# Optimization experiments

Measured on AMD Instinct MI355X. Metric: run time of the kernel, lower is better.

## Reference

```python
import jax, jax.numpy as jnp
import numpy as np

B, D = 256, 8                 # trees, tree depth (leaves at level D)
V, E, H = 32000, 128, 128     # vocab, embedding_dim, hidden_dim
N = 2 ** (D + 1) - 1          # 511 heap-indexed nodes per tree


def setup_inputs() -> dict:
    key = jax.random.key(0)
    ks = jax.random.split(key, 9)
    s = 0.05  # keep gate pre-activations in a sane range
    return {
        "tokens": jax.random.randint(ks[0], (B, N), 0, V),
        "arity": jax.random.randint(ks[1], (B, 2 ** D - 1), 0, 2).astype(jnp.int32),
        "emb": jax.random.normal(ks[2], (V, E), dtype=jnp.float32) * s,
        "W": jax.random.normal(ks[3], (4, E, H), dtype=jnp.float32) * s,      # i,f,o,u
        "bW": jax.random.normal(ks[4], (4, H), dtype=jnp.float32) * s,
        "Ubin": jax.random.normal(ks[5], (5, 2 * H, H), dtype=jnp.float32) * s,  # i,f_l,f_r,o,u
        "bUbin": jax.random.normal(ks[6], (5, H), dtype=jnp.float32) * s,
        "Uun": jax.random.normal(ks[7], (4, H, H), dtype=jnp.float32) * s,    # i,f,o,u
        "bUun": jax.random.normal(ks[8], (4, H), dtype=jnp.float32) * s,
    }


def reference(tokens, arity, emb, W, bW, Ubin, bUbin, Uun, bUun):
    # Level-synchronous bottom-up Tree-LSTM over heap-indexed perfect trees.
    x = emb[tokens]  # [B, N, E] embedding gather for every node
    depth = int(np.log2(tokens.shape[1] + 1)) - 1

    # Leaves (level `depth`): h = tanh(W_u x + b_u), c = 0
    off = 2 ** depth - 1
    lx = x[:, off:]  # [B, 2^D, E]
    h = jnp.tanh(jnp.einsum('bne,eh->bnh', lx, W[3]) + bW[3])
    c = jnp.zeros_like(h)

    for l in range(depth - 1, -1, -1):
        o2, cnt = 2 ** l - 1, 2 ** l
        nx = x[:, o2:o2 + cnt]            # [B, cnt, E] this level's tokens
        h_l, h_r = h[:, ::2], h[:, 1::2]   # children (heap order)
        c_l, c_r = c[:, ::2], c[:, 1::2]

        # Shared input projections for all 4 gates, fused into one GEMM
        Wx = jnp.einsum('bne,geh->gbnh', nx, W) + bW[:, None, None, :]
        hcat = jnp.concatenate([h_l, h_r], axis=-1)  # [B, cnt, 2H]
        Ub = jnp.einsum('bnk,gkh->gbnh', hcat, Ubin) + bUbin[:, None, None, :]
        Uu = jnp.einsum('bnh,gha->gbna', h_l, Uun) + bUun[:, None, None, :]

        # Binary branch: i, f_l, f_r (shared W_f), o, u
        i_b = jax.nn.sigmoid(Wx[0] + Ub[0])
        f_lg = jax.nn.sigmoid(Wx[1] + Ub[1])
        f_rg = jax.nn.sigmoid(Wx[1] + Ub[2])
        o_b = jax.nn.sigmoid(Wx[2] + Ub[3])
        u_b = jnp.tanh(Wx[3] + Ub[4])
        c_b = i_b * u_b + f_lg * c_l + f_rg * c_r
        h_b = o_b * jnp.tanh(c_b)

        # Unary branch (child = left child)
        i_u = jax.nn.sigmoid(Wx[0] + Uu[0])
        f_u = jax.nn.sigmoid(Wx[1] + Uu[1])
        o_u = jax.nn.sigmoid(Wx[2] + Uu[2])
        u_u = jnp.tanh(Wx[3] + Uu[3])
        c_u = i_u * u_u + f_u * c_l
        h_u = o_u * jnp.tanh(c_u)

        m = (arity[:, o2:o2 + cnt] == 1)[..., None]  # True -> binary node
        h = jnp.where(m, h_b, h_u)
        c = jnp.where(m, c_b, c_u)

    return h[:, 0], c[:, 0]  # root (h, c), each [B, H]
```

## Files before the change

### kernel.cpp

```cpp
#include <hip/hip_runtime.h>
#include <hip/hip_bf16.h>

#define NTOK 511
#define NINT 255

typedef unsigned short u16;
typedef __attribute__((ext_vector_type(8))) short bf16x8;
typedef __attribute__((ext_vector_type(4))) float f32x4;

constexpr int OFF_FLAG = 0;
constexpr int OFF_WB   = 4;
constexpr int W3B = 294912;
constexpr int WB_ELEMS = 311296;
constexpr int OFF_BIAS = OFF_WB + WB_ELEMS / 2;
constexpr int BW4 = 0, BUB4 = 512, BUB1 = 1024, BUU4 = 1152, B3 = 1664;
constexpr int BIAS_FLOATS = 1792;
constexpr int OFF_ROOT  = OFF_BIAS + BIAS_FLOATS;
constexpr int OFF_CHUNK = OFF_ROOT + 65536;
constexpr long PER_TREE = 49152;

__device__ __forceinline__ float bf2f(__hip_bfloat16 v) { return __bfloat162float(v); }
__device__ __forceinline__ short f2s(float f) {
    __hip_bfloat16 b = __float2bfloat16(f);
    return *reinterpret_cast<short*>(&b);
}
__device__ __forceinline__ float sigm(float x) { return 1.0f / (1.0f + __expf(-x)); }
__device__ __forceinline__ float tanh_(float x) { return 1.0f - 2.0f / (__expf(2.0f * x) + 1.0f); }

__device__ __forceinline__ float ldf(const void* p, long idx, int isbf) {
    return isbf ? bf2f(((const __hip_bfloat16*)p)[idx]) : ((const float*)p)[idx];
}

__device__ __forceinline__ bf16x8 ldA(const void* p, long idx, int isbf) {
    if (isbf) return *(const bf16x8*)((const short*)p + idx);
    const float* f = (const float*)p + idx;
    float4 a = *(const float4*)f, b = *(const float4*)(f + 4);
    bf16x8 r;
    r[0] = f2s(a.x); r[1] = f2s(a.y); r[2] = f2s(a.z); r[3] = f2s(a.w);
    r[4] = f2s(b.x); r[5] = f2s(b.y); r[6] = f2s(b.z); r[7] = f2s(b.w);
    return r;
}

typedef const __attribute__((address_space(1))) unsigned int* gp1_t;
typedef __attribute__((address_space(3))) unsigned int* lp3_t;
__device__ __forceinline__ void stage16(const void* g, void* l) {
    __builtin_amdgcn_global_load_lds((gp1_t)g, (lp3_t)l, 16, 0, 0);
}

__global__ void detect_kernel(const void* W, float* ws) {
    if (threadIdx.x == 0 && blockIdx.x == 0) {
        const u16* u = (const u16*)W;
        int cnt = 0;
        for (int i = 0; i < 128; i += 2) {
            u16 x = u[i];
            int ex = (x >> 7) & 0xff;
            if (x == 0 || (ex >= 96 && ex <= 127)) cnt++;
        }
        ((int*)ws)[0] = (cnt >= 48) ? 1 : 0;
    }
}

__global__ __launch_bounds__(256) void repack_mfma(
    const void* W, const void* bW, const void* Ubin, const void* bUbin,
    const void* Uun, const void* bUun, float* ws)
{
    const int isbf = ((const int*)ws)[0];
    short* wb = (short*)(ws + OFF_WB);
    float* bias = ws + OFF_BIAS;
    int tid = blockIdx.x * blockDim.x + threadIdx.x;
    int nth = gridDim.x * blockDim.x;

    for (int idx = tid; idx < 294912; idx += nth) {
        int e = idx & 511, fjc = idx >> 9;
        int jc = fjc / 72, f = fjc - jc * 72;
        int lane = e >> 3, id8 = e & 7;
        int j = jc * 16 + (lane & 15);
        float v;
        if (f < 16) {
            int g = f >> 2, ks = f & 3;
            int k = ks * 32 + (lane >> 4) * 8 + id8;
            v = ldf(W, (long)g * 16384 + k * 128 + j, isbf);
        } else if (f < 32) {
            int fu = f - 16; int g = fu >> 2, ks = fu & 3;
            int k = ks * 32 + (lane >> 4) * 8 + id8;
            v = ldf(Uun, (long)g * 16384 + k * 128 + j, isbf);
        } else {
            int fb = f - 32; int g = fb >> 3, ks = fb & 7;
            int k = ks * 32 + (lane >> 4) * 8 + id8;
            v = ldf(Ubin, (long)g * 32768 + k * 128 + j, isbf);
        }
        wb[idx] = f2s(v);
    }
    for (int idx = tid; idx < 16384; idx += nth) {
        int e = idx & 511, frag = idx >> 9;
        int jc = frag >> 2, ks = frag & 3;
        int lane = e >> 3, id8 = e & 7;
        int k = ks * 32 + (lane >> 4) * 8 + id8;
        int j = jc * 16 + (lane & 15);
        wb[W3B + idx] = f2s(ldf(W, (long)3 * 16384 + k * 128 + j, isbf));
    }
    for (int j = tid; j < 128; j += nth) {
        float4 b;
        b.x = ldf(bW, 0 * 128 + j, isbf); b.y = ldf(bW, 1 * 128 + j, isbf);
        b.z = ldf(bW, 2 * 128 + j, isbf); b.w = ldf(bW, 3 * 128 + j, isbf);
        ((float4*)(bias + BW4))[j] = b;
        float4 bb;
        bb.x = ldf(bUbin, 0 * 128 + j, isbf); bb.y = ldf(bUbin, 1 * 128 + j, isbf);
        bb.z = ldf(bUbin, 2 * 128 + j, isbf); bb.w = ldf(bUbin, 3 * 128 + j, isbf);
        ((float4*)(bias + BUB4))[j] = bb;
        (bias + BUB1)[j] = ldf(bUbin, 4 * 128 + j, isbf);
        float4 bu;
        bu.x = ldf(bUun, 0 * 128 + j, isbf); bu.y = ldf(bUun, 1 * 128 + j, isbf);
        bu.z = ldf(bUun, 2 * 128 + j, isbf); bu.w = ldf(bUun, 3 * 128 + j, isbf);
        ((float4*)(bias + BUU4))[j] = bu;
        (bias + B3)[j] = ldf(bW, 3 * 128 + j, isbf);
    }
}

#define MFMA(A, B, C) __builtin_amdgcn_mfma_f32_16x16x32_bf16(A, B, C, 0, 0, 0)

__global__ __launch_bounds__(256, 2) void leaf_mfma(
    const int* __restrict__ tokens, const void* emb, const float* __restrict__ ws,
    short* __restrict__ hOut, int treeOff, int Mtot, int iters)
{
    __shared__ short hst[4][16][132];
    const int t = threadIdx.x;
    const int isbf = ((const int*)ws)[0];
    const int wv = t >> 6, lane = t & 63, quad = lane >> 4, l16 = lane & 15;
    const short* wb = (const short*)(ws + OFF_WB);
    const float* bias = ws + OFF_BIAS;

    bf16x8 bf[32];
#pragma unroll
    for (int f = 0; f < 32; ++f)
        bf[f] = *(const bf16x8*)(wb + W3B + f * 512 + lane * 8);
    float b3v[8];
#pragma unroll
    for (int jc = 0; jc < 8; ++jc) b3v[jc] = (bias + B3)[jc * 16 + l16];

    for (int it = 0; it < iters; ++it) {
        int rb = (blockIdx.x * iters + it) * 64 + wv * 16;
        if (rb >= Mtot) break;
        int p = rb + l16; if (p >= Mtot) p = Mtot - 1;
        int bl = p >> 8, i = p & 255;
        int tk = tokens[(long)(treeOff + bl) * NTOK + 255 + i];
        bf16x8 ax[4];
#pragma unroll
        for (int ks = 0; ks < 4; ++ks)
            ax[ks] = ldA(emb, (long)tk * 128 + ks * 32 + quad * 8, isbf);
        f32x4 acc[8];
#pragma unroll
        for (int jc = 0; jc < 8; ++jc) acc[jc] = {0.f, 0.f, 0.f, 0.f};
#pragma unroll
        for (int jc = 0; jc < 8; ++jc)
#pragma unroll
            for (int ks = 0; ks < 4; ++ks)
                acc[jc] = MFMA(ax[ks], bf[jc * 4 + ks], acc[jc]);
#pragma unroll
        for (int jc = 0; jc < 8; ++jc)
#pragma unroll
            for (int r = 0; r < 4; ++r)
                hst[wv][quad * 4 + r][jc * 16 + l16] = f2s(tanh_(acc[jc][r] + b3v[jc]));
        int nloc = lane >> 2, c0 = (lane & 3) * 4;
        int prow = rb + nloc;
        if (prow < Mtot) {
#pragma unroll
            for (int jcb = 0; jcb < 8; ++jcb) {
                uint2 v = *(const uint2*)&hst[wv][nloc][jcb * 16 + c0];
                *(uint2*)&hOut[((long)jcb * Mtot + prow) * 16 + c0] = v;
            }
        }
    }
}

template <int MT>
__global__ __launch_bounds__(256, 2) void level2_mfma(
    const int* __restrict__ tokens, const int* __restrict__ arity, const void* emb,
    const float* __restrict__ ws, const short* __restrict__ hChild,
    const float* __restrict__ cChild, short* __restrict__ hOut, float* __restrict__ cOut,
    float* __restrict__ rootH, float* __restrict__ rootC,
    int lvl, int treeOff, int leafchild, int isRoot, int Mtot, int Mchild,
    int NBMB, int Q)
{
    __shared__ short Bs[72 * 512];
    __shared__ short hst[4][MT][16][20];

    constexpr int NODES = 64 * MT;
    const int t = threadIdx.x;
    const int isbf = ((const int*)ws)[0];
    const int jc = blockIdx.x / NBMB;
    const int mb = blockIdx.x - jc * NBMB;
    const int wv = t >> 6, lane = t & 63, quad = lane >> 4, l16 = lane & 15;
    const int cnt = 1 << lvl, o2 = cnt - 1;
    const short* wb = (const short*)(ws + OFF_WB);
    const float* bias = ws + OFF_BIAS;
    const short* wj = wb + (long)jc * 36864;

#pragma unroll
    for (int s = 0; s < 18; ++s) {
        int off = (s * 256 + t) * 8;
        stage16(wj + off, Bs + off);
    }

    const int j = jc * 16 + l16;
    const float4 bw = ((const float4*)(bias + BW4))[j];
    const float4 bb = ((const float4*)(bias + BUB4))[j];
    const float  b1 = (bias + BUB1)[j];
    const float4 bu = ((const float4*)(bias + BUU4))[j];

    __syncthreads();

    for (int q = 0; q < Q; ++q) {
        const int p0 = (mb * Q + q) * NODES;
        if (p0 >= Mtot) break;

        bf16x8 ax[MT][4], ah[MT][8];
#pragma unroll
        for (int mt = 0; mt < MT; ++mt) {
            int row = wv * (16 * MT) + mt * 16 + l16;
            int p = p0 + row; if (p >= Mtot) p = Mtot - 1;
            int bl = p >> lvl, i = p - (bl << lvl);
            long crow = (long)bl * (cnt << 1) + 2 * i;
            int tk = tokens[(long)(treeOff + bl) * NTOK + o2 + i];
#pragma unroll
            for (int ks = 0; ks < 4; ++ks)
                ax[mt][ks] = ldA(emb, (long)tk * 128 + ks * 32 + quad * 8, isbf);
#pragma unroll
            for (int ks = 0; ks < 8; ++ks) {
                int k0 = ks * 32 + quad * 8;
                int side = k0 >> 7, kl = k0 & 127;
                ah[mt][ks] = *(const bf16x8*)(hChild +
                    ((long)(kl >> 4) * Mchild + crow + side) * 16 + (kl & 15));
            }
        }

        int arv[MT][4];
        float clv[MT][4], crv[MT][4];
#pragma unroll
        for (int mt = 0; mt < MT; ++mt)
#pragma unroll
        for (int r = 0; r < 4; ++r) {
            int pe = p0 + wv * (16 * MT) + mt * 16 + quad * 4 + r;
            if (pe >= Mtot) pe = Mtot - 1;
            int ble = pe >> lvl, ie = pe - (ble << lvl);
            arv[mt][r] = arity[(long)(treeOff + ble) * NINT + o2 + ie];
            if (!leafchild) {
                long crowe = (long)ble * (cnt << 1) + 2 * ie;
                clv[mt][r] = cChild[((long)jc * Mchild + crowe) * 16 + l16];
                crv[mt][r] = cChild[((long)jc * Mchild + crowe + 1) * 16 + l16];
            } else { clv[mt][r] = 0.f; crv[mt][r] = 0.f; }
        }

        f32x4 aW[4][MT], aU[4][MT], aB[5][MT];
#pragma unroll
        for (int g = 0; g < 4; ++g)
#pragma unroll
            for (int mt = 0; mt < MT; ++mt) { aW[g][mt] = {0,0,0,0}; aU[g][mt] = {0,0,0,0}; }
#pragma unroll
        for (int g = 0; g < 5; ++g)
#pragma unroll
            for (int mt = 0; mt < MT; ++mt) aB[g][mt] = {0,0,0,0};

#pragma unroll
        for (int f = 0; f < 16; ++f) {
            bf16x8 b = *(const bf16x8*)&Bs[f * 512 + lane * 8];
#pragma unroll
            for (int mt = 0; mt < MT; ++mt)
                aW[f >> 2][mt] = MFMA(ax[mt][f & 3], b, aW[f >> 2][mt]);
        }
#pragma unroll
        for (int f = 16; f < 32; ++f) {
            bf16x8 b = *(const bf16x8*)&Bs[f * 512 + lane * 8];
            int g = (f - 16) >> 2, ks = (f - 16) & 3;
#pragma unroll
            for (int mt = 0; mt < MT; ++mt)
                aU[g][mt] = MFMA(ah[mt][ks], b, aU[g][mt]);
        }
#pragma unroll
        for (int f = 32; f < 72; ++f) {
            bf16x8 b = *(const bf16x8*)&Bs[f * 512 + lane * 8];
            int fb = f - 32, g = fb >> 3, ks = fb & 7;
#pragma unroll
            for (int mt = 0; mt < MT; ++mt)
                aB[g][mt] = MFMA(ah[mt][ks], b, aB[g][mt]);
        }

#pragma unroll
        for (int mt = 0; mt < MT; ++mt) {
#pragma unroll
            for (int r = 0; r < 4; ++r) {
                int ml = wv * (16 * MT) + mt * 16 + quad * 4 + r;
                int p = p0 + ml;
                bool val = (p < Mtot);
                int pc = val ? p : Mtot - 1;
                int bl = pc >> lvl;
                bool bin = (arv[mt][r] == 1);
                float w0 = aW[0][mt][r] + bw.x;
                float w1 = aW[1][mt][r] + bw.y;
                float w2 = aW[2][mt][r] + bw.z;
                float w3 = aW[3][mt][r] + bw.w;
                float pi, pf, po, pu;
                if (bin) { pi = w0 + aB[0][mt][r] + bb.x; pf = w1 + aB[1][mt][r] + bb.y;
                           po = w2 + aB[3][mt][r] + bb.w; pu = w3 + aB[4][mt][r] + b1; }
                else     { pi = w0 + aU[0][mt][r] + bu.x; pf = w1 + aU[1][mt][r] + bu.y;
                           po = w2 + aU[2][mt][r] + bu.z; pu = w3 + aU[3][mt][r] + bu.w; }
                float cl = clv[mt][r];
                float cr = bin ? crv[mt][r] : 0.f;
                float frv = bin ? sigm(w1 + aB[2][mt][r] + bb.z) : 0.f;
                float ig = sigm(pi), fg = sigm(pf), og = sigm(po), ug = tanh_(pu);
                float c = ig * ug + fg * cl + frv * cr;
                float h = og * tanh_(c);
                if (isRoot) {
                    if (val) {
                        rootH[(long)(treeOff + bl) * 128 + j] = h;
                        rootC[(long)(treeOff + bl) * 128 + j] = c;
                    }
                } else {
                    if (val) cOut[((long)jc * Mtot + pc) * 16 + l16] = c;
                    hst[wv][mt][quad * 4 + r][l16] = f2s(h);
                }
            }
        }
        if (!isRoot) {
            int nloc = lane >> 2, c0 = (lane & 3) * 4;
#pragma unroll
            for (int mt = 0; mt < MT; ++mt) {
                int prow = p0 + wv * (16 * MT) + mt * 16 + nloc;
                if (prow < Mtot) {
                    uint2 v = *(const uint2*)&hst[wv][mt][nloc][c0];
                    *(uint2*)&hOut[((long)jc * Mtot + prow) * 16 + c0] = v;
                }
            }
        }
    }
}

__global__ __launch_bounds__(256) void out_kernel(const float* ws, void* out)
{
    const int isbf = ((const int*)ws)[0];
    const float* rootH = ws + OFF_ROOT;
    const float* rootC = rootH + 32768;
    int t = blockIdx.x * 256 + threadIdx.x;
    float h = rootH[t], c = rootC[t];
    if (isbf) {
        ((__hip_bfloat16*)out)[t]         = __float2bfloat16(h);
        ((__hip_bfloat16*)out)[32768 + t] = __float2bfloat16(c);
    } else {
        ((float*)out)[t]         = h;
        ((float*)out)[32768 + t] = c;
    }
}

extern "C" void kernel_launch(void* const* d_in, const int* in_sizes, int n_in,
                              void* d_out, int out_size, void* d_ws, size_t ws_size,
                              hipStream_t stream)
{
    const int* tokens = (const int*)d_in[0];
    const int* arity  = (const int*)d_in[1];
    const void* emb   = d_in[2];
    const void* W     = d_in[3];
    const void* bW    = d_in[4];
    const void* Ubin  = d_in[5];
    const void* bUbin = d_in[6];
    const void* Uun   = d_in[7];
    const void* bUun  = d_in[8];

    float* ws = (float*)d_ws;

    int Bc = 256;
    while (Bc > 1 && (size_t)(OFF_CHUNK + Bc * PER_TREE) * 4 > ws_size) Bc >>= 1;
    const int nCh = 256 / Bc;

    detect_kernel<<<1, 64, 0, stream>>>(W, ws);
    repack_mfma<<<128, 256, 0, stream>>>(W, bW, Ubin, bUbin, Uun, bUun, ws);

    short* Ha = (short*)(ws + OFF_CHUNK);
    short* Hb = Ha + (long)Bc * 32768;
    float* Ca = (float*)(Hb + (long)Bc * 16384);
    float* Cb = Ca + (long)Bc * 8192;
    float* rootH = ws + OFF_ROOT;
    float* rootC = rootH + 32768;

    for (int cidx = 0; cidx < nCh; ++cidx) {
        int toff = cidx * Bc;
        {
            int Mleaf = Bc * 256;
            int NBL = (Mleaf + 63) / 64; if (NBL > 512) NBL = 512;
            int itersL = (Mleaf + NBL * 64 - 1) / (NBL * 64);
            leaf_mfma<<<NBL, 256, 0, stream>>>(tokens, emb, ws, Ha, toff, Mleaf, itersL);
        }
        for (int l = 7; l >= 0; --l) {
            int M = Bc << l;
            int Mchild = Bc << (l + 1);
            const short* hC = (l & 1) ? Ha : Hb;
            const float* cC = (l & 1) ? Ca : Cb;
            short* hO = (l & 1) ? Hb : Ha;
            float* cO = (l & 1) ? Cb : Ca;
            int lc = (l == 7) ? 1 : 0;
            int isRoot = (l == 0) ? 1 : 0;
            if (l >= 5) {
                int NBM = (M + 127) / 128;
                int Q = (NBM + 63) / 64;
                int NBMB = (NBM + Q - 1) / Q;
                level2_mfma<2><<<dim3(NBMB * 8), 256, 0, stream>>>(
                    tokens, arity, emb, ws, hC, cC, hO, cO, rootH, rootC,
                    l, toff, lc, isRoot, M, Mchild, NBMB, Q);
            } else {
                int NBM = (M + 63) / 64;
                level2_mfma<1><<<dim3(NBM * 8), 256, 0, stream>>>(
                    tokens, arity, emb, ws, hC, cC, hO, cO, rootH, rootC,
                    l, toff, lc, isRoot, M, Mchild, NBM, 1);
            }
        }
    }
    out_kernel<<<128, 256, 0, stream>>>(ws, d_out);
}
```

Before: 164.8 us.

## Fuse top five tree levels into one per-tree kernel with LDS state

Levels 4 through 0 are replaced by a single tail kernel with one block per tree. It keeps child h and c in double-buffered shared memory and reads weights directly from global memory, which removes five launches and their global round trips for the small upper levels. The remaining levels 7..5 now use a single-tile (MT=1) kernel with a different grid split. The cost is that the tail runs few blocks with little parallelism and fetches weights from global/L2 at every level.

```diff
diff --git a/kernel.cpp b/kernel.cpp
--- a/kernel.cpp
+++ b/kernel.cpp
@@ -173,19 +173,16 @@
     }
 }
 
-template <int MT>
 __global__ __launch_bounds__(256, 2) void level2_mfma(
     const int* __restrict__ tokens, const int* __restrict__ arity, const void* emb,
     const float* __restrict__ ws, const short* __restrict__ hChild,
     const float* __restrict__ cChild, short* __restrict__ hOut, float* __restrict__ cOut,
-    float* __restrict__ rootH, float* __restrict__ rootC,
-    int lvl, int treeOff, int leafchild, int isRoot, int Mtot, int Mchild,
+    int lvl, int treeOff, int leafchild, int Mtot, int Mchild,
     int NBMB, int Q)
 {
     __shared__ short Bs[72 * 512];
-    __shared__ short hst[4][MT][16][20];
-
-    constexpr int NODES = 64 * MT;
+    __shared__ short hst[4][16][20];
+
     const int t = threadIdx.x;
     const int isbf = ((const int*)ws)[0];
     const int jc = blockIdx.x / NBMB;
@@ -211,127 +208,217 @@
     __syncthreads();
 
     for (int q = 0; q < Q; ++q) {
-        const int p0 = (mb * Q + q) * NODES;
+        const int p0 = (mb * Q + q) * 64;
         if (p0 >= Mtot) break;
 
-        bf16x8 ax[MT][4], ah[MT][8];
-#pragma unroll
-        for (int mt = 0; mt < MT; ++mt) {
-            int row = wv * (16 * MT) + mt * 16 + l16;
-            int p = p0 + row; if (p >= Mtot) p = Mtot - 1;
-            int bl = p >> lvl, i = p - (bl << lvl);
-            long crow = (long)bl * (cnt << 1) + 2 * i;
-            int tk = tokens[(long)(treeOff + bl) * NTOK + o2 + i];
-#pragma unroll
-            for (int ks = 0; ks < 4; ++ks)
-                ax[mt][ks] = ldA(emb, (long)tk * 128 + ks * 32 + quad * 8, isbf);
-#pragma unroll
-            for (int ks = 0; ks < 8; ++ks) {
-                int k0 = ks * 32 + quad * 8;
-                int side = k0 >> 7, kl = k0 & 127;
-                ah[mt][ks] = *(const bf16x8*)(hChild +
-                    ((long)(kl >> 4) * Mchild + crow + side) * 16 + (kl & 15));
-            }
-        }
-
-        int arv[MT][4];
-        float clv[MT][4], crv[MT][4];
-#pragma unroll
-        for (int mt = 0; mt < MT; ++mt)
+        int row = wv * 16 + l16;
+        int p = p0 + row; if (p >= Mtot) p = Mtot - 1;
+        int bl = p >> lvl, i = p - (bl << lvl);
+        long crow = (long)bl * (cnt << 1) + 2 * i;
+        int tk = tokens[(long)(treeOff + bl) * NTOK + o2 + i];
+        bf16x8 ax[4], ah[8];
+#pragma unroll
+        for (int ks = 0; ks < 4; ++ks)
+            ax[ks] = ldA(emb, (long)tk * 128 + ks * 32 + quad * 8, isbf);
+#pragma unroll
+        for (int ks = 0; ks < 8; ++ks) {
+            int k0 = ks * 32 + quad * 8;
+            int side = k0 >> 7, kl = k0 & 127;
+            ah[ks] = *(const bf16x8*)(hChild +
+                ((long)(kl >> 4) * Mchild + crow + side) * 16 + (kl & 15));
+        }
+
+        f32x4 aW[4], aU[4], aB[5];
+#pragma unroll
+        for (int g = 0; g < 4; ++g) { aW[g] = {0,0,0,0}; aU[g] = {0,0,0,0}; }
+#pragma unroll
+        for (int g = 0; g < 5; ++g) aB[g] = {0,0,0,0};
+
+#pragma unroll
+        for (int f = 0; f < 16; ++f) {
+            bf16x8 b = *(const bf16x8*)&Bs[f * 512 + lane * 8];
+            aW[f >> 2] = MFMA(ax[f & 3], b, aW[f >> 2]);
+        }
+#pragma unroll
+        for (int f = 16; f < 32; ++f) {
+            bf16x8 b = *(const bf16x8*)&Bs[f * 512 + lane * 8];
+            aU[(f - 16) >> 2] = MFMA(ah[(f - 16) & 3], b, aU[(f - 16) >> 2]);
+        }
+#pragma unroll
+        for (int f = 32; f < 72; ++f) {
+            bf16x8 b = *(const bf16x8*)&Bs[f * 512 + lane * 8];
+            int fb = f - 32;
+            aB[fb >> 3] = MFMA(ah[fb & 7], b, aB[fb >> 3]);
+        }
+
+        int arv[4]; float clv[4], crv[4];
 #pragma unroll
         for (int r = 0; r < 4; ++r) {
-            int pe = p0 + wv * (16 * MT) + mt * 16 + quad * 4 + r;
+            int pe = p0 + wv * 16 + quad * 4 + r;
             if (pe >= Mtot) pe = Mtot - 1;
             int ble = pe >> lvl, ie = pe - (ble << lvl);
-            arv[mt][r] = arity[(long)(treeOff + ble) * NINT + o2 + ie];
+            arv[r] = arity[(long)(treeOff + ble) * NINT + o2 + ie];
             if (!leafchild) {
                 long crowe = (long)ble * (cnt << 1) + 2 * ie;
-                clv[mt][r] = cChild[((long)jc * Mchild + crowe) * 16 + l16];
-                crv[mt][r] = cChild[((long)jc * Mchild + crowe + 1) * 16 + l16];
-            } else { clv[mt][r] = 0.f; crv[mt][r] = 0.f; }
-        }
-
-        f32x4 aW[4][MT], aU[4][MT], aB[5][MT];
-#pragma unroll
-        for (int g = 0; g < 4; ++g)
-#pragma unroll
-            for (int mt = 0; mt < MT; ++mt) { aW[g][mt] = {0,0,0,0}; aU[g][mt] = {0,0,0,0}; }
-#pragma unroll
-        for (int g = 0; g < 5; ++g)
-#pragma unroll
-            for (int mt = 0; mt < MT; ++mt) aB[g][mt] = {0,0,0,0};
-
-#pragma unroll
-        for (int f = 0; f < 16; ++f) {
-            bf16x8 b = *(const bf16x8*)&Bs[f * 512 + lane * 8];
-#pragma unroll
-            for (int mt = 0; mt < MT; ++mt)
-                aW[f >> 2][mt] = MFMA(ax[mt][f & 3], b, aW[f >> 2][mt]);
-        }
-#pragma unroll
-        for (int f = 16; f < 32; ++f) {
-            bf16x8 b = *(const bf16x8*)&Bs[f * 512 + lane * 8];
-            int g = (f - 16) >> 2, ks = (f - 16) & 3;
-#pragma unroll
-            for (int mt = 0; mt < MT; ++mt)
-                aU[g][mt] = MFMA(ah[mt][ks], b, aU[g][mt]);
-        }
-#pragma unroll
-        for (int f = 32; f < 72; ++f) {
-            bf16x8 b = *(const bf16x8*)&Bs[f * 512 + lane * 8];
-            int fb = f - 32, g = fb >> 3, ks = fb & 7;
-#pragma unroll
-            for (int mt = 0; mt < MT; ++mt)
-                aB[g][mt] = MFMA(ah[mt][ks], b, aB[g][mt]);
-        }
-
-#pragma unroll
-        for (int mt = 0; mt < MT; ++mt) {
+                clv[r] = cChild[((long)jc * Mchild + crowe) * 16 + l16];
+                crv[r] = cChild[((long)jc * Mchild + crowe + 1) * 16 + l16];
+            } else { clv[r] = 0.f; crv[r] = 0.f; }
+        }
+
+#pragma unroll
+        for (int r = 0; r < 4; ++r) {
+            int ml = wv * 16 + quad * 4 + r;
+            int pr = p0 + ml;
+            bool val = (pr < Mtot);
+            int pc = val ? pr : Mtot - 1;
+            bool bin = (arv[r] == 1);
+            float w0 = aW[0][r] + bw.x;
+            float w1 = aW[1][r] + bw.y;
+            float w2 = aW[2][r] + bw.z;
+            float w3 = aW[3][r] + bw.w;
+            float pi, pf, po, pu;
+            if (bin) { pi = w0 + aB[0][r] + bb.x; pf = w1 + aB[1][r] + bb.y;
+                       po = w2 + aB[3][r] + bb.w; pu = w3 + aB[4][r] + b1; }
+            else     { pi = w0 + aU[0][r] + bu.x; pf = w1 + aU[1][r] + bu.y;
+                       po = w2 + aU[2][r] + bu.z; pu = w3 + aU[3][r] + bu.w; }
+            float cl = clv[r];
+            float cr = bin ? crv[r] : 0.f;
+            float frv = bin ? sigm(w1 + aB[2][r] + bb.z) : 0.f;
+            float ig = sigm(pi), fg = sigm(pf), og = sigm(po), ug = tanh_(pu);
+            float c = ig * ug + fg * cl + frv * cr;
+            float h = og * tanh_(c);
+            if (val) cOut[((long)jc * Mtot + pc) * 16 + l16] = c;
+            hst[wv][quad * 4 + r][l16] = f2s(h);
+        }
+        {
+            int nloc = lane >> 2, c0 = (lane & 3) * 4;
+            int prow = p0 + wv * 16 + nloc;
+            if (prow < Mtot) {
+                uint2 v = *(const uint2*)&hst[wv][nloc][c0];
+                *(uint2*)&hOut[((long)jc * Mtot + prow) * 16 + c0] = v;
+            }
+        }
+    }
+}
+
+__global__ __launch_bounds__(256, 2) void tail_mfma(
+    const int* __restrict__ tokens, const int* __restrict__ arity, const void* emb,
+    const float* __restrict__ ws, const short* __restrict__ hChild,
+    const float* __restrict__ cChild, float* __restrict__ rootH, float* __restrict__ rootC,
+    int treeOff, int Mchild4)
+{
+    __shared__ short hb[2][8 * 16 * 20];
+    __shared__ float cb[2][8 * 16 * 20];
+
+    const int t = threadIdx.x;
+    const int isbf = ((const int*)ws)[0];
+    const int bl = blockIdx.x;
+    const int wv = t >> 6, lane = t & 63, quad = lane >> 4, l16 = lane & 15;
+    const short* wb = (const short*)(ws + OFF_WB);
+    const float* bias = ws + OFF_BIAS;
+    const long tB = (long)(treeOff + bl) * NTOK;
+    const long tA = (long)(treeOff + bl) * NINT;
+
+    int cur = 0;
+    for (int l = 4; l >= 0; --l) {
+        const int cnt = 1 << l, o2 = cnt - 1;
+        int i = (l16 < cnt) ? l16 : cnt - 1;
+        int tk = tokens[tB + o2 + i];
+        bf16x8 ax[4], ah[8];
+#pragma unroll
+        for (int ks = 0; ks < 4; ++ks)
+            ax[ks] = ldA(emb, (long)tk * 128 + ks * 32 + quad * 8, isbf);
+        if (l == 4) {
+            long crow = (long)bl * 32 + 2 * i;
+#pragma unroll
+            for (int ks = 0; ks < 8; ++ks) {
+                int k0 = ks * 32 + quad * 8, side = k0 >> 7, kl = k0 & 127;
+                ah[ks] = *(const bf16x8*)(hChild +
+                    ((long)(kl >> 4) * Mchild4 + crow + side) * 16 + (kl & 15));
+            }
+        } else {
+            int crow = 2 * i;
+#pragma unroll
+            for (int ks = 0; ks < 8; ++ks) {
+                int k0 = ks * 32 + quad * 8, side = k0 >> 7, kl = k0 & 127;
+                ah[ks] = *(const bf16x8*)&hb[cur][(kl >> 4) * 320 + (crow + side) * 20 + (kl & 15)];
+            }
+        }
+        for (int jx = 0; jx < 2; ++jx) {
+            const int jc = wv * 2 + jx;
+            const short* wj = wb + (long)jc * 36864;
+            const int j = jc * 16 + l16;
+            const float4 bw = ((const float4*)(bias + BW4))[j];
+            const float4 bb = ((const float4*)(bias + BUB4))[j];
+            const float  b1 = (bias + BUB1)[j];
+            const float4 bu = ((const float4*)(bias + BUU4))[j];
+
+            f32x4 aW[4], aU[4], aB[5];
+#pragma unroll
+            for (int g = 0; g < 4; ++g) { aW[g] = {0,0,0,0}; aU[g] = {0,0,0,0}; }
+#pragma unroll
+            for (int g = 0; g < 5; ++g) aB[g] = {0,0,0,0};
+
+#pragma unroll
+            for (int f = 0; f < 16; ++f) {
+                bf16x8 b = *(const bf16x8*)(wj + f * 512 + lane * 8);
+                aW[f >> 2] = MFMA(ax[f & 3], b, aW[f >> 2]);
+            }
+#pragma unroll
+            for (int f = 16; f < 32; ++f) {
+                bf16x8 b = *(const bf16x8*)(wj + f * 512 + lane * 8);
+                aU[(f - 16) >> 2] = MFMA(ah[(f - 16) & 3], b, aU[(f - 16) >> 2]);
+            }
+#pragma unroll
+            for (int f = 32; f < 72; ++f) {
+                bf16x8 b = *(const bf16x8*)(wj + f * 512 + lane * 8);
+                int fb = f - 32;
+                aB[fb >> 3] = MFMA(ah[fb & 7], b, aB[fb >> 3]);
+            }
+
 #pragma unroll
             for (int r = 0; r < 4; ++r) {
-                int ml = wv * (16 * MT) + mt * 16 + quad * 4 + r;
-                int p = p0 + ml;
-                bool val = (p < Mtot);
-                int pc = val ? p : Mtot - 1;
-                int bl = pc >> lvl;
-                bool bin = (arv[mt][r] == 1);
-                float w0 = aW[0][mt][r] + bw.x;
-                float w1 = aW[1][mt][r] + bw.y;
-                float w2 = aW[2][mt][r] + bw.z;
-                float w3 = aW[3][mt][r] + bw.w;
+                int node = quad * 4 + r;
+                int ie = (node < cnt) ? node : cnt - 1;
+                int arvv = arity[tA + o2 + ie];
+                float cl, cr;
+                if (l == 4) {
+                    long crowe = (long)bl * 32 + 2 * ie;
+                    cl = cChild[((long)jc * Mchild4 + crowe) * 16 + l16];
+                    cr = cChild[((long)jc * Mchild4 + crowe + 1) * 16 + l16];
+                } else {
+                    int crowe = 2 * ie;
+                    cl = cb[cur][jc * 320 + crowe * 20 + l16];
+                    cr = cb[cur][jc * 320 + (crowe + 1) * 20 + l16];
+                }
+                bool bin = (arvv == 1);
+                float w0 = aW[0][r] + bw.x;
+                float w1 = aW[1][r] + bw.y;
+                float w2 = aW[2][r] + bw.z;
+                float w3 = aW[3][r] + bw.w;
                 float pi, pf, po, pu;
-                if (bin) { pi = w0 + aB[0][mt][r] + bb.x; pf = w1 + aB[1][mt][r] + bb.y;
-                           po = w2 + aB[3][mt][r] + bb.w; pu = w3 + aB[4][mt][r] + b1; }
-                else     { pi = w0 + aU[0][mt][r] + bu.x; pf = w1 + aU[1][mt][r] + bu.y;
-                           po = w2 + aU[2][mt][r] + bu.z; pu = w3 + aU[3][mt][r] + bu.w; }
-                float cl = clv[mt][r];
-                float cr = bin ? crv[mt][r] : 0.f;
-                float frv = bin ? sigm(w1 + aB[2][mt][r] + bb.z) : 0.f;
+                if (bin) { pi = w0 + aB[0][r] + bb.x; pf = w1 + aB[1][r] + bb.y;
+                           po = w2 + aB[3][r] + bb.w; pu = w3 + aB[4][r] + b1; }
+                else     { pi = w0 + aU[0][r] + bu.x; pf = w1 + aU[1][r] + bu.y;
+                           po = w2 + aU[2][r] + bu.z; pu = w3 + aU[3][r] + bu.w; }
+                if (!bin) cr = 0.f;
+                float frv = bin ? sigm(w1 + aB[2][r] + bb.z) : 0.f;
                 float ig = sigm(pi), fg = sigm(pf), og = sigm(po), ug = tanh_(pu);
                 float c = ig * ug + fg * cl + frv * cr;
                 float h = og * tanh_(c);
-                if (isRoot) {
-                    if (val) {
+                if (l == 0) {
+                    if (node == 0) {
                         rootH[(long)(treeOff + bl) * 128 + j] = h;
                         rootC[(long)(treeOff + bl) * 128 + j] = c;
                     }
-                } else {
-                    if (val) cOut[((long)jc * Mtot + pc) * 16 + l16] = c;
-                    hst[wv][mt][quad * 4 + r][l16] = f2s(h);
+                } else if (node < cnt) {
+                    hb[cur ^ 1][jc * 320 + node * 20 + l16] = f2s(h);
+                    cb[cur ^ 1][jc * 320 + node * 20 + l16] = c;
                 }
             }
         }
-        if (!isRoot) {
-            int nloc = lane >> 2, c0 = (lane & 3) * 4;
-#pragma unroll
-            for (int mt = 0; mt < MT; ++mt) {
-                int prow = p0 + wv * (16 * MT) + mt * 16 + nloc;
-                if (prow < Mtot) {
-                    uint2 v = *(const uint2*)&hst[wv][mt][nloc][c0];
-                    *(uint2*)&hOut[((long)jc * Mtot + prow) * 16 + c0] = v;
-                }
-            }
-        }
+        __syncthreads();
+        cur ^= 1;
     }
 }
 
@@ -389,7 +476,7 @@
             int itersL = (Mleaf + NBL * 64 - 1) / (NBL * 64);
             leaf_mfma<<<NBL, 256, 0, stream>>>(tokens, emb, ws, Ha, toff, Mleaf, itersL);
         }
-        for (int l = 7; l >= 0; --l) {
+        for (int l = 7; l >= 5; --l) {
             int M = Bc << l;
             int Mchild = Bc << (l + 1);
             const short* hC = (l & 1) ? Ha : Hb;
@@ -397,21 +484,15 @@
             short* hO = (l & 1) ? Hb : Ha;
             float* cO = (l & 1) ? Cb : Ca;
             int lc = (l == 7) ? 1 : 0;
-            int isRoot = (l == 0) ? 1 : 0;
-            if (l >= 5) {
-                int NBM = (M + 127) / 128;
-                int Q = (NBM + 63) / 64;
-                int NBMB = (NBM + Q - 1) / Q;
-                level2_mfma<2><<<dim3(NBMB * 8), 256, 0, stream>>>(
-                    tokens, arity, emb, ws, hC, cC, hO, cO, rootH, rootC,
-                    l, toff, lc, isRoot, M, Mchild, NBMB, Q);
-            } else {
-                int NBM = (M + 63) / 64;
-                level2_mfma<1><<<dim3(NBM * 8), 256, 0, stream>>>(
-                    tokens, arity, emb, ws, hC, cC, hO, cO, rootH, rootC,
-                    l, toff, lc, isRoot, M, Mchild, NBM, 1);
-            }
-        }
+            int NBM = (M + 63) / 64;
+            int Q = (NBM + 127) / 128;
+            int NBMB = (NBM + Q - 1) / Q;
+            level2_mfma<<<dim3(NBMB * 8), 256, 0, stream>>>(
+                tokens, arity, emb, ws, hC, cC, hO, cO,
+                l, toff, lc, M, Mchild, NBMB, Q);
+        }
+        tail_mfma<<<dim3(Bc), 256, 0, stream>>>(
+            tokens, arity, emb, ws, Hb, Cb, rootH, rootC, toff, Bc << 5);
     }
     out_kernel<<<128, 256, 0, stream>>>(ws, d_out);
 }
```

Result: slower. 183.5 us (+11.4%).
